# Performance work log

Measured on AMD Instinct MI355X. Metric: run time of the kernel, lower is better.

The kernel has to match this reference:

```python
import jax, jax.numpy as jnp
import numpy as np

N = 500_000
D = 128
NUM_SEGMENTS = 4096


def setup_inputs() -> dict:
    key = jax.random.key(0)
    k1, k2, k3 = jax.random.split(key, 3)
    feat = jax.random.normal(k1, (N, D), dtype=jnp.float32)
    # xavier_uniform for Linear(D -> 1): bound = sqrt(6 / (D + 1))
    bound = float(np.sqrt(6.0 / (D + 1)))
    gate_w = jax.random.uniform(k2, (D, 1), dtype=jnp.float32, minval=-bound, maxval=bound)
    gate_b = jnp.zeros((1,), dtype=jnp.float32)
    segment_ids = jnp.sort(jax.random.randint(k3, (N,), 0, NUM_SEGMENTS, dtype=jnp.int64))
    return {
        "feat": feat,
        "gate_w": gate_w,
        "gate_b": gate_b,
        "segment_ids": segment_ids,
        "num_segments": NUM_SEGMENTS,
    }


def reference(feat, gate_w, gate_b, segment_ids, num_segments):
    # gate_nn: Linear(D -> 1), gate shape [N, 1] -> squeeze to [N]
    gate = (feat @ gate_w + gate_b)[:, 0]                      # [N]
    # segment softmax over nodes of each graph (stable)
    seg_max = jax.ops.segment_max(gate, segment_ids, num_segments=num_segments)  # [G]
    e = jnp.exp(gate - seg_max[segment_ids])                   # [N]
    denom = jax.ops.segment_sum(e, segment_ids, num_segments=num_segments)       # [G]
    alpha = e / denom[segment_ids]                             # [N]
    # weighted segment sum readout: [G, D]
    readout = jax.ops.segment_sum(feat * alpha[:, None], segment_ids,
                                  num_segments=num_segments)
    return readout
```

## Files before the change

kernel.cpp:

```cpp
#include <hip/hip_runtime.h>
#include <math.h>

#define NSEG 4096
#define DD   128

typedef float f4 __attribute__((ext_vector_type(4)));

__device__ __forceinline__ int lower_bound(const int* __restrict__ seg, int N, int g) {
    int lo = 0, hi = N;
    while (lo < hi) {
        int mid = (lo + hi) >> 1;
        if (seg[mid] < g) lo = mid + 1; else hi = mid;
    }
    return lo;
}

__global__ __launch_bounds__(256) void fused_kernel(
        const float* __restrict__ feat,
        const float* __restrict__ gw,
        const float* __restrict__ gb,
        const int*  __restrict__ seg,
        int N,
        float* __restrict__ out) {
    __shared__ float gs[2][32];
    __shared__ f4    red[8][32];

    int g = blockIdx.x;
    int s = lower_bound(seg, N, g);
    int e = lower_bound(seg, N, g + 1);
    int len = e - s;

    int tid = threadIdx.x;
    int rg  = tid >> 5;
    int c   = tid & 31;

    const f4* fp = (const f4*)feat;
    f4    w4 = ((const f4*)gw)[c];
    float b0 = gb[0];

    float m = -INFINITY, l = 0.0f;
    f4 acc = {0.f, 0.f, 0.f, 0.f};

    int ntiles = (len + 31) >> 5;

    f4 va = {0,0,0,0}, vb = {0,0,0,0}, vc = {0,0,0,0}, vd = {0,0,0,0};
    {
        int n1 = s + rg;
        if (n1      < e) va = __builtin_nontemporal_load(&fp[(n1     ) * 32 + c]);
        if (n1 + 8  < e) vb = __builtin_nontemporal_load(&fp[(n1 + 8 ) * 32 + c]);
        if (n1 + 16 < e) vc = __builtin_nontemporal_load(&fp[(n1 + 16) * 32 + c]);
        if (n1 + 24 < e) vd = __builtin_nontemporal_load(&fp[(n1 + 24) * 32 + c]);
    }

    for (int t = 0; t < ntiles; ++t) {
        int base = s + t * 32;
        int n1 = base + rg;
        f4 ca = va, cb = vb, cc = vc, cd = vd;

        int p1 = n1 + 32;
        va = (f4){0,0,0,0}; vb = (f4){0,0,0,0}; vc = (f4){0,0,0,0}; vd = (f4){0,0,0,0};
        if (p1      < e) va = __builtin_nontemporal_load(&fp[(p1     ) * 32 + c]);
        if (p1 + 8  < e) vb = __builtin_nontemporal_load(&fp[(p1 + 8 ) * 32 + c]);
        if (p1 + 16 < e) vc = __builtin_nontemporal_load(&fp[(p1 + 16) * 32 + c]);
        if (p1 + 24 < e) vd = __builtin_nontemporal_load(&fp[(p1 + 24) * 32 + c]);

        float d1 = ca.x*w4.x + ca.y*w4.y + ca.z*w4.z + ca.w*w4.w;
        float d2 = cb.x*w4.x + cb.y*w4.y + cb.z*w4.z + cb.w*w4.w;
        float d3 = cc.x*w4.x + cc.y*w4.y + cc.z*w4.z + cc.w*w4.w;
        float d4 = cd.x*w4.x + cd.y*w4.y + cd.z*w4.z + cd.w*w4.w;
        #pragma unroll
        for (int off = 16; off; off >>= 1) {
            d1 += __shfl_xor(d1, off);
            d2 += __shfl_xor(d2, off);
            d3 += __shfl_xor(d3, off);
            d4 += __shfl_xor(d4, off);
        }
        int buf = t & 1;
        if (c == 0) {
            gs[buf][rg]      = (n1      < e) ? d1 + b0 : -INFINITY;
            gs[buf][rg + 8]  = (n1 + 8  < e) ? d2 + b0 : -INFINITY;
            gs[buf][rg + 16] = (n1 + 16 < e) ? d3 + b0 : -INFINITY;
            gs[buf][rg + 24] = (n1 + 24 < e) ? d4 + b0 : -INFINITY;
        }
        __syncthreads();

        float gj = gs[buf][tid & 31];
        float tmax = gj;
        #pragma unroll
        for (int off = 16; off; off >>= 1) tmax = fmaxf(tmax, __shfl_xor(tmax, off));
        float m_new = fmaxf(m, tmax);
        float scale = __expf(m - m_new);
        float pj = __expf(gj - m_new);
        float psum = pj;
        #pragma unroll
        for (int off = 16; off; off >>= 1) psum += __shfl_xor(psum, off);
        l = l * scale + psum;

        float pa = __expf(gs[buf][rg]      - m_new);
        float pb = __expf(gs[buf][rg + 8]  - m_new);
        float pc = __expf(gs[buf][rg + 16] - m_new);
        float pd = __expf(gs[buf][rg + 24] - m_new);
        acc = acc * scale + pa * ca + pb * cb + pc * cc + pd * cd;
        m = m_new;
    }

    red[rg][c] = acc;
    __syncthreads();
    if (rg == 0) {
        f4 r = red[0][c];
        #pragma unroll
        for (int k = 1; k < 8; ++k) r += red[k][c];
        float invl = (len > 0) ? 1.0f / l : 0.0f;
        r *= invl;
        ((f4*)out)[g * 32 + c] = r;
    }
}

extern "C" void kernel_launch(void* const* d_in, const int* in_sizes, int n_in,
                              void* d_out, int out_size, void* d_ws, size_t ws_size,
                              hipStream_t stream) {
    const float* feat = (const float*)d_in[0];
    const float* gw   = (const float*)d_in[1];
    const float* gb   = (const float*)d_in[2];
    const int*   seg  = (const int*)d_in[3];
    int N = in_sizes[0] / DD;

    fused_kernel<<<NSEG, 256, 0, stream>>>(feat, gw, gb, seg, N, (float*)d_out);
}
```

Baseline: 50.69 us.

## Use per-warp online softmax state to remove per-tile block barrier

Each 32-lane row group now keeps its own running max and sum over its own rows, so the shared gate buffer and the __syncthreads in every tile go away. The per-group states are merged once at the end with rescaled weights. Loads are clamped to the last valid row, which removes the bounds branches, and empty segments exit early. This adds a final cross-group rescale and some redundant loads at the tail of each segment.

```diff
diff --git a/kernel.cpp b/kernel.cpp
--- a/kernel.cpp
+++ b/kernel.cpp
@@ -3,6 +3,7 @@
 
 #define NSEG 4096
 #define DD   128
+#define NEG  (-1e30f)
 
 typedef float f4 __attribute__((ext_vector_type(4)));
 
@@ -22,8 +23,9 @@
         const int*  __restrict__ seg,
         int N,
         float* __restrict__ out) {
-    __shared__ float gs[2][32];
     __shared__ f4    red[8][32];
+    __shared__ float mred[8];
+    __shared__ float lred[8];
 
     int g = blockIdx.x;
     int s = lower_bound(seg, N, g);
@@ -34,83 +36,80 @@
     int rg  = tid >> 5;
     int c   = tid & 31;
 
+    if (len <= 0) {
+        if (rg == 0) ((f4*)out)[g * 32 + c] = (f4){0.f, 0.f, 0.f, 0.f};
+        return;
+    }
+
     const f4* fp = (const f4*)feat;
     f4    w4 = ((const f4*)gw)[c];
     float b0 = gb[0];
 
-    float m = -INFINITY, l = 0.0f;
+    float m = NEG, l = 0.0f;
     f4 acc = {0.f, 0.f, 0.f, 0.f};
 
     int ntiles = (len + 31) >> 5;
+    int emax = e - 1;
 
-    f4 va = {0,0,0,0}, vb = {0,0,0,0}, vc = {0,0,0,0}, vd = {0,0,0,0};
-    {
-        int n1 = s + rg;
-        if (n1      < e) va = __builtin_nontemporal_load(&fp[(n1     ) * 32 + c]);
-        if (n1 + 8  < e) vb = __builtin_nontemporal_load(&fp[(n1 + 8 ) * 32 + c]);
-        if (n1 + 16 < e) vc = __builtin_nontemporal_load(&fp[(n1 + 16) * 32 + c]);
-        if (n1 + 24 < e) vd = __builtin_nontemporal_load(&fp[(n1 + 24) * 32 + c]);
-    }
+    int n0 = s + rg;
+    f4 nv0 = __builtin_nontemporal_load(&fp[min(n0,      emax) * 32 + c]);
+    f4 nv1 = __builtin_nontemporal_load(&fp[min(n0 + 8,  emax) * 32 + c]);
+    f4 nv2 = __builtin_nontemporal_load(&fp[min(n0 + 16, emax) * 32 + c]);
+    f4 nv3 = __builtin_nontemporal_load(&fp[min(n0 + 24, emax) * 32 + c]);
 
     for (int t = 0; t < ntiles; ++t) {
-        int base = s + t * 32;
-        int n1 = base + rg;
-        f4 ca = va, cb = vb, cc = vc, cd = vd;
+        int r0 = s + t * 32 + rg;
+        f4 c0 = nv0, c1 = nv1, c2 = nv2, c3 = nv3;
 
-        int p1 = n1 + 32;
-        va = (f4){0,0,0,0}; vb = (f4){0,0,0,0}; vc = (f4){0,0,0,0}; vd = (f4){0,0,0,0};
-        if (p1      < e) va = __builtin_nontemporal_load(&fp[(p1     ) * 32 + c]);
-        if (p1 + 8  < e) vb = __builtin_nontemporal_load(&fp[(p1 + 8 ) * 32 + c]);
-        if (p1 + 16 < e) vc = __builtin_nontemporal_load(&fp[(p1 + 16) * 32 + c]);
-        if (p1 + 24 < e) vd = __builtin_nontemporal_load(&fp[(p1 + 24) * 32 + c]);
+        int p0 = r0 + 32;
+        nv0 = __builtin_nontemporal_load(&fp[min(p0,      emax) * 32 + c]);
+        nv1 = __builtin_nontemporal_load(&fp[min(p0 + 8,  emax) * 32 + c]);
+        nv2 = __builtin_nontemporal_load(&fp[min(p0 + 16, emax) * 32 + c]);
+        nv3 = __builtin_nontemporal_load(&fp[min(p0 + 24, emax) * 32 + c]);
 
-        float d1 = ca.x*w4.x + ca.y*w4.y + ca.z*w4.z + ca.w*w4.w;
-        float d2 = cb.x*w4.x + cb.y*w4.y + cb.z*w4.z + cb.w*w4.w;
-        float d3 = cc.x*w4.x + cc.y*w4.y + cc.z*w4.z + cc.w*w4.w;
-        float d4 = cd.x*w4.x + cd.y*w4.y + cd.z*w4.z + cd.w*w4.w;
+        float d0 = c0.x*w4.x + c0.y*w4.y + c0.z*w4.z + c0.w*w4.w;
+        float d1 = c1.x*w4.x + c1.y*w4.y + c1.z*w4.z + c1.w*w4.w;
+        float d2 = c2.x*w4.x + c2.y*w4.y + c2.z*w4.z + c2.w*w4.w;
+        float d3 = c3.x*w4.x + c3.y*w4.y + c3.z*w4.z + c3.w*w4.w;
         #pragma unroll
         for (int off = 16; off; off >>= 1) {
+            d0 += __shfl_xor(d0, off);
             d1 += __shfl_xor(d1, off);
             d2 += __shfl_xor(d2, off);
             d3 += __shfl_xor(d3, off);
-            d4 += __shfl_xor(d4, off);
         }
-        int buf = t & 1;
-        if (c == 0) {
-            gs[buf][rg]      = (n1      < e) ? d1 + b0 : -INFINITY;
-            gs[buf][rg + 8]  = (n1 + 8  < e) ? d2 + b0 : -INFINITY;
-            gs[buf][rg + 16] = (n1 + 16 < e) ? d3 + b0 : -INFINITY;
-            gs[buf][rg + 24] = (n1 + 24 < e) ? d4 + b0 : -INFINITY;
-        }
-        __syncthreads();
+        float g0 = (r0      < e) ? d0 + b0 : NEG;
+        float g1 = (r0 + 8  < e) ? d1 + b0 : NEG;
+        float g2 = (r0 + 16 < e) ? d2 + b0 : NEG;
+        float g3 = (r0 + 24 < e) ? d3 + b0 : NEG;
 
-        float gj = gs[buf][tid & 31];
-        float tmax = gj;
-        #pragma unroll
-        for (int off = 16; off; off >>= 1) tmax = fmaxf(tmax, __shfl_xor(tmax, off));
-        float m_new = fmaxf(m, tmax);
+        float m_new = fmaxf(m, fmaxf(fmaxf(g0, g1), fmaxf(g2, g3)));
         float scale = __expf(m - m_new);
-        float pj = __expf(gj - m_new);
-        float psum = pj;
-        #pragma unroll
-        for (int off = 16; off; off >>= 1) psum += __shfl_xor(psum, off);
-        l = l * scale + psum;
-
-        float pa = __expf(gs[buf][rg]      - m_new);
-        float pb = __expf(gs[buf][rg + 8]  - m_new);
-        float pc = __expf(gs[buf][rg + 16] - m_new);
-        float pd = __expf(gs[buf][rg + 24] - m_new);
-        acc = acc * scale + pa * ca + pb * cb + pc * cc + pd * cd;
+        float p0w = __expf(g0 - m_new);
+        float p1w = __expf(g1 - m_new);
+        float p2w = __expf(g2 - m_new);
+        float p3w = __expf(g3 - m_new);
+        l = l * scale + (p0w + p1w) + (p2w + p3w);
+        acc = acc * scale + p0w * c0 + p1w * c1 + p2w * c2 + p3w * c3;
         m = m_new;
     }
 
     red[rg][c] = acc;
+    if (c == 0) { mred[rg] = m; lred[rg] = l; }
     __syncthreads();
     if (rg == 0) {
-        f4 r = red[0][c];
+        float M = mred[0];
         #pragma unroll
-        for (int k = 1; k < 8; ++k) r += red[k][c];
-        float invl = (len > 0) ? 1.0f / l : 0.0f;
+        for (int k = 1; k < 8; ++k) M = fmaxf(M, mred[k]);
+        f4 r = {0.f, 0.f, 0.f, 0.f};
+        float ltot = 0.0f;
+        #pragma unroll
+        for (int k = 0; k < 8; ++k) {
+            float wgt = __expf(mred[k] - M);
+            ltot += lred[k] * wgt;
+            r += wgt * red[k][c];
+        }
+        float invl = 1.0f / ltot;
         r *= invl;
         ((f4*)out)[g * 32 + c] = r;
     }
```

New measurement: 46.53 us. -8.2%, faster.
